# Optimization experiments

Hardware: AMD Instinct MI355X
Metric: run time of the kernel (lower is better)

Reference implementation:

```python
import jax, jax.numpy as jnp
import numpy as np

N_SAMPLES = 65536
N_OSC = 16
N_RES = 16
CPD = 16
EXPR = 2
WIN = 2048
FRAMES = 512
DEF_FRAMES = 256


def fft_convolve(a, b):
    n = a.shape[-1]
    pa = jnp.pad(a, [(0, 0)] * (a.ndim - 1) + [(0, a.shape[-1])])
    pb = jnp.pad(b, [(0, 0)] * (b.ndim - 1) + [(0, b.shape[-1])])
    spec = jnp.fft.rfft(pa, axis=-1) * jnp.fft.rfft(pb, axis=-1)
    return jnp.fft.irfft(spec, axis=-1)[..., :n]


def make_ramp(n, ramp_length=10):
    return jnp.ones(n, dtype=jnp.float32).at[:ramp_length].set(jnp.linspace(0.0, 1.0, ramp_length, dtype=jnp.float32))


def setup_inputs() -> dict:
    key = jax.random.key(0)
    ks = jax.random.split(key, 12)
    u = lambda k, shape, lo, hi: jax.random.uniform(k, shape, jnp.float32, lo, hi)
    return {
        'control_signal': jax.random.normal(ks[0], (1, 1, CPD, FRAMES), jnp.float32),
        'deformations': jax.random.normal(ks[1], (1, 1, EXPR, DEF_FRAMES), jnp.float32),
        'noise': u(ks[2], (CPD, WIN), -1.0, 1.0),
        'attack_envelopes': u(ks[3], (CPD, WIN), -1.0, 1.0),
        'router': u(ks[4], (CPD, N_RES), -1.0, 1.0),
        'mix': u(ks[5], (N_RES, 2), -1.0, 1.0),
        'gains': u(ks[6], (N_RES, 1), 0.01, 1.1),
        'damping': u(ks[7], (N_OSC, N_RES, EXPR), 0.5, 1.5),
        'mass': u(ks[8], (N_OSC, N_RES, EXPR), -2.0, 2.0),
        'tension': u(ks[9], (N_OSC, N_RES, EXPR), 4.0, 9.0),
        'initial_displacement': u(ks[10], (N_OSC, N_RES, EXPR), -1.0, 2.0),
        'amplitudes': u(ks[11], (N_OSC, N_RES, EXPR, 1), -1.0, 1.0),
    }


def _materialize_resonances(damping, mass, tension, initial_displacement, amplitudes):
    time = jnp.linspace(0.0, 10.0, N_SAMPLES, dtype=jnp.float32).reshape(1, 1, 1, N_SAMPLES)
    m = jax.nn.sigmoid(mass)[..., None]
    dmp = jax.nn.sigmoid(damping)[..., None] * 30.0
    ten = 10.0 ** tension[..., None]
    x0 = initial_displacement[..., None]
    xd = dmp / (2.0 * m)
    omega = jnp.sqrt(jnp.clip(ten - xd ** 2, 1e-12, None))
    phi = jnp.arctan2(xd * x0, x0 * omega)  # initial_velocity = 0
    a = x0 / jnp.cos(phi)
    z = a * jnp.exp(-xd * time) * jnp.cos(omega * time - phi)  # (osc, res, expr, N)
    res = jnp.sum(z * amplitudes ** 2, axis=0)  # (res, expr, N)
    res = res[None, None] * make_ramp(N_SAMPLES)  # (1,1,res,expr,N)
    return res


def _forward(control_signal, deformations, noise, attack_envelopes, router, mix, gains,
             damping, mass, tension, initial_displacement, amplitudes):
    res = _materialize_resonances(damping, mass, tension, initial_displacement, amplitudes)
    res = res / (jnp.linalg.norm(res, axis=-1, keepdims=True) + 1e-8)  # unit_norm

    # routing matmul: (b,e,frames,cpd) @ (cpd,res) -> permuted back
    routed = jnp.einsum('becf,cr->berf', control_signal, router)  # (1,1,res,frames)
    before_upsample = routed

    # sparse zero-hole upsampling
    factor = N_SAMPLES // FRAMES
    up = jnp.zeros((1, 1, N_RES, 1, N_SAMPLES), control_signal.dtype)
    up = up.at[..., ::factor].set(routed[:, :, :, None, :])

    # attack envelopes: shape == window_size fast path -> elementwise noise multiply
    impulse = attack_envelopes * noise
    impulse = jnp.pad(impulse, ((0, 0), (0, N_SAMPLES - WIN)))  # ensure_last_axis_length
    impulse = impulse.reshape(1, 1, CPD, 1, N_SAMPLES)

    routed_c = fft_convolve(impulse, up)  # (1,1,16,1,N)
    cs = jnp.sum(routed_c.reshape(1, CPD, N_SAMPLES), axis=1, keepdims=True)  # (1,1,N)

    conv = fft_convolve(routed_c, res)  # (1,1,res,expr,N)

    base = jnp.zeros_like(deformations).at[:, :, 0:1, :].set(1.0)
    d = jax.nn.softmax(base + deformations, axis=-2)  # (1,1,expr,DF)
    d = d.reshape(1, 1, 1, EXPR, DEF_FRAMES)
    d = jax.image.resize(d, (1, 1, 1, EXPR, N_SAMPLES), method='linear')

    x = jnp.sum(d * conv, axis=-2)  # (1,1,res,N)

    mixes = jax.nn.softmax(mix.reshape(1, 1, N_RES, 1, 1, 2), axis=-1)
    stacked = jnp.stack([routed_c, x.reshape(routed_c.shape)], axis=-1)  # (1,1,res,1,N,2)
    x = jnp.sum(mixes * stacked, axis=-1)  # (1,1,res,1,N)
    x = x.reshape(1, 1, N_RES, N_SAMPLES)

    summed = jnp.tanh(x * jnp.abs(gains.reshape(1, 1, N_RES, 1)))
    summed = jnp.sum(summed, axis=-2, keepdims=True)  # (1,1,1,N)
    return summed, before_upsample, cs


def reference(control_signal, deformations, noise, attack_envelopes, router, mix, gains,
              damping, mass, tension, initial_displacement, amplitudes):
    return _forward(control_signal, deformations, noise, attack_envelopes, router, mix, gains,
                    damping, mass, tension, initial_displacement, amplitudes)
```

## Files before the change

### kernel.cpp

```cpp
#include <hip/hip_runtime.h>
#include <hip/hip_bf16.h>
#include <math.h>

#define N_SAMPLES 65536
#define N_OSC 16
#define N_RES 16
#define CPD 16
#define EXPR 2
#define WIN 2048
#define FRAMES 512
#define DEF_FRAMES 256
#define NRE 32
#define R1TILE 1024
#define R1TILES (N_SAMPLES / R1TILE)

#define MBLK 4096
#define RSTRIDE 67648
#define WSZ 6176
#define NSTEP 65

#define M_RES 2048
#define M_CONV 3072
#define M_AF (M_CONV + NSTEP)
#define M_TOTAL (M_AF + 64)

typedef __hip_bfloat16 bf16;
typedef __attribute__((ext_vector_type(8))) _Float16 half8v;
typedef __attribute__((ext_vector_type(4))) float f32x4;
typedef __attribute__((ext_vector_type(4))) unsigned short ushort4v;
typedef __attribute__((ext_vector_type(8))) unsigned short ushort8v;

static __device__ __forceinline__ float ldv(const void* p, int i, int f32f) {
    if (f32f) return ((const float*)p)[i];
    return __bfloat162float(((const bf16*)p)[i]);
}
static __device__ __forceinline__ void stv(void* p, int i, float v, int f32f) {
    if (f32f) ((float*)p)[i] = v;
    else      ((bf16*)p)[i] = __float2bfloat16(v);
}
static __device__ __forceinline__ unsigned short f2h(float f) {
    union { _Float16 h; unsigned short u; } a; a.h = (_Float16)f; return a.u;
}

#define OUT_SUM_OFF 0
#define OUT_ROUTED_OFF 65536
#define OUT_CS_OFF 73728

#define DT_F64 (10.0 / 65535.0)
#define INV2PI 0.15915494309189535

__global__ __launch_bounds__(256) void prep_kernel(
    const void* ctrl, const void* defo, const void* noise, const void* attack,
    const void* router, const void* mix, const void* gains,
    const void* damping, const void* mass, const void* tension,
    const void* x0in, const void* amps,
    double* par, float* impulse, float* routed, float* dcur, float* mixg,
    int* rsup, int* nbound, int* gflag, float* sumf, void* out)
{
    int tid = threadIdx.x;
    int b = blockIdx.x;
    __shared__ int sbad;
    if (tid == 0) sbad = 0;
    __syncthreads();
    {
        const bf16* tb = (const bf16*)tension;
        int bad = 0;
        for (int i = tid; i < N_OSC * N_RES * EXPR; i += 256) {
            float v = __bfloat162float(tb[i]);
            if (!(v > 3.0f && v < 10.0f)) bad = 1;
        }
        if (bad) sbad = 1;
    }
    __syncthreads();
    const int f32f = sbad;

    if (b < 32) {
        int r = b >> 1;
        int f = ((b & 1) << 8) + tid;
        float s = 0.f;
#pragma unroll
        for (int c = 0; c < CPD; ++c)
            s += ldv(ctrl, c * FRAMES + f, f32f) * ldv(router, c * N_RES + r, f32f);
        int i = r * FRAMES + f;
        routed[i] = s;
        stv(out, OUT_ROUTED_OFF + i, s, f32f);
    } else if (b < 64) {
        int base = (b - 32) * 1024 + tid * 4;
#pragma unroll
        for (int j = 0; j < 4; ++j) {
            int i = base + j;
            impulse[i] = ldv(attack, i, f32f) * ldv(noise, i, f32f);
        }
    } else if (b == 64) {
        int i = tid;
        if (i < DEF_FRAMES) {
            float a0 = 1.0f + ldv(defo, i, f32f);
            float a1 = ldv(defo, DEF_FRAMES + i, f32f);
            float mx = fmaxf(a0, a1);
            float e0 = expf(a0 - mx), e1 = expf(a1 - mx);
            float inv = 1.0f / (e0 + e1);
            dcur[i] = e0 * inv;
            dcur[DEF_FRAMES + i] = e1 * inv;
        }
    } else if (b == 65) {
        if (tid < N_RES) {
            int r = tid;
            float a0 = ldv(mix, 2 * r, f32f), a1 = ldv(mix, 2 * r + 1, f32f);
            float mx = fmaxf(a0, a1);
            float e0 = expf(a0 - mx), e1 = expf(a1 - mx);
            float inv = 1.0f / (e0 + e1);
            mixg[r] = e0 * inv; mixg[16 + r] = e1 * inv;
            mixg[32 + r] = fabsf(ldv(gains, r, f32f));
        }
        if (tid < NRE) rsup[tid] = 0;
        if (tid == 0) gflag[0] = f32f;
    } else if (b < 98) {
        int re = b - 66;
        __shared__ double s_xd[16];
        if (tid < 16) {
            int o = tid;
            int i = o * 32 + re;
            double mm  = 1.0 / (1.0 + exp(-(double)ldv(mass, i, f32f)));
            double dmp = 30.0 / (1.0 + exp(-(double)ldv(damping, i, f32f)));
            double ten = pow(10.0, (double)ldv(tension, i, f32f));
            double x0  = (double)ldv(x0in, i, f32f);
            double amp = (double)ldv(amps, i, f32f);
            double xd  = dmp / (2.0 * mm);
            double om2 = ten - xd * xd;
            if (om2 < 1e-12) om2 = 1e-12;
            double om  = sqrt(om2);
            double phi = atan2(xd * x0, x0 * om);
            double a   = (x0 == 0.0) ? 0.0 : x0 / cos(phi);
            int p = re * 16 + o;
            par[p] = xd; par[512 + p] = om; par[1024 + p] = phi; par[1536 + p] = a * amp * amp;
            s_xd[o] = xd;
        }
        __syncthreads();
        if (tid == 0) {
            double mt = 0.0;
            for (int o = 0; o < 16; ++o) {
                double t = 35.0 / s_xd[o];
                if (t > mt) mt = t;
            }
            int nb = (int)(mt * 6553.5) + 1;
            if (nb > N_SAMPLES - 1) nb = N_SAMPLES - 1;
            nbound[re] = nb;
        }
    } else {
        ((float4*)sumf)[(b - 98) * 256 + tid] = float4{0.f, 0.f, 0.f, 0.f};
    }
}

__global__ __launch_bounds__(256) void mid_kernel(
    const double* par, const int* nbound, double* dssq_part, int* rsup,
    unsigned short* res_rev, const float* impulse, const float* routed,
    float* routed_c, unsigned short* afrag, unsigned short* rfrag)
{
    int b = blockIdx.x;
    int tid = threadIdx.x;
    if (b < M_RES) {
        int re = b >> 6, tile = b & 63;
        int n0 = tile * R1TILE;
        unsigned short* rrc = res_rev + (size_t)re * RSTRIDE;
        if (tile == R1TILES - 1) {
            ushort8v z = {0,0,0,0,0,0,0,0};
            for (int i = tid * 8; i < RSTRIDE - N_SAMPLES; i += 2048)
                *(ushort8v*)&rrc[N_SAMPLES + i] = z;
        }
        if (n0 > nbound[re]) {
            ushort8v z = {0,0,0,0,0,0,0,0};
            *(ushort8v*)&rrc[(N_SAMPLES - n0 - R1TILE) + tid * 8] = z;
            if (tid == 0) dssq_part[re * R1TILES + tile] = 0.0;
            return;
        }
        __shared__ double s_om[16], s_phi[16], s_xd[16], s_coef[16];
        __shared__ float s_drev[16], s_decf[16];
        if (tid < 16) {
            int pi = re * 16 + tid;
            double xd = par[pi], om = par[512 + pi];
            s_xd[tid] = xd; s_om[tid] = om;
            s_phi[tid] = par[1024 + pi]; s_coef[tid] = par[1536 + pi];
            s_drev[tid] = (float)(om * DT_F64 * INV2PI);
            s_decf[tid] = (float)exp(-xd * DT_F64);
        }
        __syncthreads();
        int ns = n0 + tid * 4;
        double t0 = (double)ns * DT_F64;
        float p[16], cd[16], drev[16], decf[16];
#pragma unroll
        for (int o = 0; o < 16; ++o) {
            double arg = s_om[o] * t0 - s_phi[o];
            double rev = arg * INV2PI;
            rev -= rint(rev);
            p[o] = (float)rev;
            cd[o] = (float)s_coef[o] * expf((float)(-s_xd[o] * t0));
            drev[o] = s_drev[o]; decf[o] = s_decf[o];
        }
        float vals[4];
        double ssq = 0.0;
#pragma unroll
        for (int j = 0; j < 4; ++j) {
            float acc = 0.f;
#pragma unroll
            for (int o = 0; o < 16; ++o) {
                acc += cd[o] * __builtin_amdgcn_cosf(p[o]);
                cd[o] *= decf[o];
                float pn = p[o] + drev[o];
                p[o] = pn - floorf(pn);
            }
            int n = ns + j;
            if (n < 10) acc *= (float)n * (1.0f / 9.0f);
            vals[j] = acc;
            ssq += (double)acc * (double)acc;
        }
        unsigned short u0 = f2h(vals[0]), u1 = f2h(vals[1]);
        unsigned short u2 = f2h(vals[2]), u3 = f2h(vals[3]);
        ushort4v o4 = { u3, u2, u1, u0 };
        *(ushort4v*)&rrc[(N_SAMPLES - 4) - ns] = o4;
        int mi = 0;
        if ((unsigned short)(u0 << 1)) mi = ns;
        if ((unsigned short)(u1 << 1)) mi = ns + 1;
        if ((unsigned short)(u2 << 1)) mi = ns + 2;
        if ((unsigned short)(u3 << 1)) mi = ns + 3;
        __shared__ int ib[256];
        __shared__ double rb[256];
        ib[tid] = mi; rb[tid] = ssq; __syncthreads();
        for (int st = 128; st > 0; st >>= 1) {
            if (tid < st) { ib[tid] = max(ib[tid], ib[tid + st]); rb[tid] += rb[tid + st]; }
            __syncthreads();
        }
        if (tid == 0) {
            dssq_part[re * R1TILES + tile] = rb[0];
            if (ib[0] > 0) atomicMax(&rsup[re], ib[0]);
        }
        return;
    }
    if (b < M_CONV) {
        int cb = b - M_RES;
        int c = cb >> 6;
        int n0 = (cb & 63) << 10;
        int q0 = n0 >> 7;
        __shared__ float imp_s[WIN];
        __shared__ float ro_s[24];
        {
            const float4* src = (const float4*)(impulse + c * WIN);
            float4* dst = (float4*)imp_s;
#pragma unroll
            for (int k = 0; k < 2; ++k) dst[tid + 256 * k] = src[tid + 256 * k];
            if (tid < 23) {
                int k = q0 - 15 + tid;
                ro_s[tid] = (k >= 0) ? routed[c * FRAMES + k] : 0.0f;
            }
        }
        __syncthreads();
        int s4 = (4 * tid) & 127;
        int qi = tid >> 5;
        float a0 = 0.f, a1 = 0.f, a2 = 0.f, a3 = 0.f;
#pragma unroll
        for (int dk = 0; dk < 16; ++dk) {
            float rv = ro_s[qi + 15 - dk];
            float4 iv = *(const float4*)&imp_s[s4 + (dk << 7)];
            a0 += rv * iv.x; a1 += rv * iv.y; a2 += rv * iv.z; a3 += rv * iv.w;
        }
        *(float4*)&routed_c[(size_t)c * N_SAMPLES + n0 + 4 * tid] = float4{a0, a1, a2, a3};
        return;
    }
    if (b < M_AF) {
        int t = b - M_CONV;
        for (int idx = tid; idx < 16 * 512; idx += 256) {
            int ch = idx >> 9, r = idx & 511;
            int lane = r >> 3, s = r & 7;
            int k = 32 * t + ((lane >> 4) << 3) + s - (lane & 15);
            float v = (k >= 0 && k < WIN) ? impulse[ch * WIN + k] : 0.0f;
            afrag[(size_t)((ch * NSTEP + t) * 64 + lane) * 8 + s] = f2h(v);
        }
        return;
    }
    {
        int bb = b - M_AF;
        for (int idx = bb * 4096 + tid; idx < bb * 4096 + 4096; idx += 256) {
            int ss = idx & 7, ln = (idx >> 3) & 63, v = (idx >> 9) & 31, r = idx >> 14;
            int k = 16 * v + (ln & 15) - 8 * (ln >> 4) - ss;
            float val = (k >= 0 && k < FRAMES) ? routed[r * FRAMES + k] : 0.0f;
            rfrag[idx] = f2h(val);
        }
    }
}

__global__ __launch_bounds__(256) void fir_kernel(const unsigned short* res_rev,
                                                  const unsigned short* afrag,
                                                  const int* rsup, const double* dssq_part,
                                                  unsigned short* ghT)
{
    int re = blockIdx.y;
    int mb = blockIdx.x * MBLK;
    int tid = threadIdx.x;
    int rs = rsup[re];
    int d0 = mb >> 7;
    unsigned short* ghc = ghT + (size_t)re * N_SAMPLES;
    if (mb > rs + (WIN - 1)) {
        int s = tid >> 1, h = tid & 1;
        ushort8v z = {0,0,0,0,0,0,0,0};
        size_t o = (size_t)s * 512 + d0 + 16 * h;
        *(ushort8v*)&ghc[o] = z;
        *(ushort8v*)&ghc[o + 8] = z;
        return;
    }
    __shared__ unsigned short W[WSZ];
    __shared__ double s_in[64];
    __shared__ float s_invf;
    if (tid < 64) s_in[tid] = dssq_part[re * R1TILES + tid];
    {
        const unsigned short* src = res_rev + (size_t)re * RSTRIDE + (N_SAMPLES - MBLK - mb);
        for (int i = tid * 8; i < WSZ; i += 2048)
            *(ushort8v*)&W[i] = *(const ushort8v*)&src[i];
    }
    __syncthreads();
    if (tid == 0) {
        double s = 0.0;
#pragma unroll
        for (int i = 0; i < 64; ++i) s += s_in[i];
        s_invf = (float)(1.0 / (sqrt(s) + 1e-8));
    }

    int w = tid >> 6, lane = tid & 63;
    int j = lane & 15, g = lane >> 4;
    const unsigned short* af = afrag + (size_t)(re >> 1) * (NSTEP * 512) + lane * 8;

    int c00 = mb + 1024 * w + 15;
    int c01 = c00 + 256, c02 = c00 + 512, c03 = c00 + 768;
    int tlo0 = max(0, (c00 - rs) >> 5), tlo1 = max(0, (c01 - rs) >> 5);
    int tlo2 = max(0, (c02 - rs) >> 5), tlo3 = max(0, (c03 - rs) >> 5);
    int thi0 = min(NSTEP - 1, (c00 + 240) >> 5), thi1 = min(NSTEP - 1, (c01 + 240) >> 5);
    int thi2 = min(NSTEP - 1, (c02 + 240) >> 5), thi3 = min(NSTEP - 1, (c03 + 240) >> 5);
    int tmin = tlo0, tmax = thi3;

    f32x4 acc0 = {0.f,0.f,0.f,0.f}, acc1 = acc0, acc2 = acc0, acc3 = acc0;
    int xbase = 4080 - 1024 * w - 16 * j + 8 * g;

    half8v afr = {};
    if (tmin <= tmax) afr = *(const half8v*)(af + (size_t)tmin * 512);
    for (int t = tmin; t <= tmax; ++t) {
        half8v acur = afr;
        if (t < tmax) afr = *(const half8v*)(af + (size_t)(t + 1) * 512);
        int xt = xbase + 32 * t;
        if (t >= tlo0 && t <= thi0)
            acc0 = __builtin_amdgcn_mfma_f32_16x16x32_f16(acur, *(const half8v*)&W[xt],       acc0, 0, 0, 0);
        if (t >= tlo1 && t <= thi1)
            acc1 = __builtin_amdgcn_mfma_f32_16x16x32_f16(acur, *(const half8v*)&W[xt - 256], acc1, 0, 0, 0);
        if (t >= tlo2 && t <= thi2)
            acc2 = __builtin_amdgcn_mfma_f32_16x16x32_f16(acur, *(const half8v*)&W[xt - 512], acc2, 0, 0, 0);
        if (t >= tlo3 && t <= thi3)
            acc3 = __builtin_amdgcn_mfma_f32_16x16x32_f16(acur, *(const half8v*)&W[xt - 768], acc3, 0, 0, 0);
    }

    __syncthreads();
    float invf = s_invf;
    unsigned short* T = W;
    int base_nm = 1024 * w + 16 * j + 15 - 4 * g;
#define WT(ACC, AA) { \
    int nm0_ = base_nm + 256 * (AA); \
    T[((nm0_    ) & 127) * 37 + ((nm0_    ) >> 7)] = f2h(ACC[0] * invf); \
    T[((nm0_ - 1) & 127) * 37 + ((nm0_ - 1) >> 7)] = f2h(ACC[1] * invf); \
    T[((nm0_ - 2) & 127) * 37 + ((nm0_ - 2) >> 7)] = f2h(ACC[2] * invf); \
    T[((nm0_ - 3) & 127) * 37 + ((nm0_ - 3) >> 7)] = f2h(ACC[3] * invf); }
    WT(acc0, 0) WT(acc1, 1) WT(acc2, 2) WT(acc3, 3)
#undef WT
    __syncthreads();
    {
        int s = tid >> 1, h = tid & 1;
        const unsigned short* Tr = T + s * 37 + 16 * h;
        ushort8v o0, o1;
#pragma unroll
        for (int k = 0; k < 8; ++k) { o0[k] = Tr[k]; o1[k] = Tr[8 + k]; }
        size_t o = (size_t)s * 512 + d0 + 16 * h;
        *(ushort8v*)&ghc[o] = o0;
        *(ushort8v*)&ghc[o + 8] = o1;
    }
}

__global__ __launch_bounds__(256) void conv2_kernel(const unsigned short* ghT,
        const unsigned short* rfrag, const float* routed_c, const float* dcur,
        const float* mixg, const int* rsup, float* sumf)
{
    __shared__ float xbuf[4][2048];
    __shared__ float dcur_s[2 * DEF_FRAMES];
    __shared__ float mix_s[48];
    int tid = threadIdx.x;
    int qt = blockIdx.x, rg = blockIdx.y;
    int q0 = qt * 16;
    int w = tid >> 6, lane = tid & 63;
    int j = lane & 15, gq = lane >> 4;
    int re = rg * 4 + w;
    int r = re >> 1, e = re & 1;

    if (tid < 48) mix_s[tid] = mixg[tid];
    for (int i = tid; i < 2 * DEF_FRAMES; i += 256) dcur_s[i] = dcur[i];
    __syncthreads();

    int tmax = (q0 + 15) >> 5;
    int sup = rsup[re] + (WIN - 1);
    int tend = min(tmax, sup >> 12);

    f32x4 acc[8];
#pragma unroll
    for (int st = 0; st < 8; ++st) acc[st] = f32x4{0.f, 0.f, 0.f, 0.f};

    const unsigned short* rfb = rfrag + ((size_t)r * 32 * 64 + lane) * 8;
    const unsigned short* gT = ghT + (size_t)re * N_SAMPLES;
    for (int t = 0; t <= tend; ++t) {
        int v = (q0 - 32 * t) >> 4;
        half8v a = *(const half8v*)(rfb + (size_t)v * 512);
        int bofs = j * 512 + 8 * gq + 32 * t;
#pragma unroll
        for (int st = 0; st < 8; ++st)
            acc[st] = __builtin_amdgcn_mfma_f32_16x16x32_f16(
                a, *(const half8v*)(gT + bofs + st * 8192), acc[st], 0, 0, 0);
    }

    float* xb = xbuf[w];
    const float* dc = dcur_s + DEF_FRAMES * e;
#pragma unroll
    for (int st = 0; st < 8; ++st) {
#pragma unroll
        for (int p = 0; p < 4; ++p) {
            int nl = 128 * (4 * gq + p) + 16 * st + j;
            int n = 128 * q0 + nl;
            float xc = ((float)n + 0.5f) * (1.0f / 256.0f) - 0.5f;
            float fl = floorf(xc);
            int i0 = (int)fl;
            float wfr = xc - fl;
            int ia = min(max(i0, 0), DEF_FRAMES - 1);
            int ib2 = min(max(i0 + 1, 0), DEF_FRAMES - 1);
            float de = dc[ia] * (1.0f - wfr) + dc[ib2] * wfr;
            xb[nl] = acc[st][p] * de;
        }
    }
    __syncthreads();

    int r0 = rg * 2, r1 = rg * 2 + 1;
    float m00 = mix_s[r0], m01 = mix_s[16 + r0], g0s = mix_s[32 + r0];
    float m10 = mix_s[r1], m11 = mix_s[16 + r1], g1s = mix_s[32 + r1];
    const float* rc0 = routed_c + (size_t)r0 * N_SAMPLES + 128 * q0;
    const float* rc1 = routed_c + (size_t)r1 * N_SAMPLES + 128 * q0;
    float* sf = sumf + 128 * q0;
    for (int nl = tid; nl < 2048; nl += 256) {
        float xr0 = xbuf[0][nl] + xbuf[1][nl];
        float xr1 = xbuf[2][nl] + xbuf[3][nl];
        float xf0 = m00 * rc0[nl] + m01 * xr0;
        float xf1 = m10 * rc1[nl] + m11 * xr1;
        atomicAdd(&sf[nl], tanhf(xf0 * g0s) + tanhf(xf1 * g1s));
    }
}

__global__ __launch_bounds__(256) void final2_kernel(const float* sumf, const float* routed_c,
                                                     const int* gflag, void* out)
{
    int f32f = gflag[0];
    int n = (blockIdx.x * 256 + threadIdx.x) * 4;
    float4 v = *(const float4*)(sumf + n);
    stv(out, OUT_SUM_OFF + n,     v.x, f32f);
    stv(out, OUT_SUM_OFF + n + 1, v.y, f32f);
    stv(out, OUT_SUM_OFF + n + 2, v.z, f32f);
    stv(out, OUT_SUM_OFF + n + 3, v.w, f32f);
    float c0 = 0.f, c1 = 0.f, c2 = 0.f, c3 = 0.f;
#pragma unroll
    for (int c = 0; c < CPD; ++c) {
        float4 t = *(const float4*)(routed_c + (size_t)c * N_SAMPLES + n);
        c0 += t.x; c1 += t.y; c2 += t.z; c3 += t.w;
    }
    stv(out, OUT_CS_OFF + n,     c0, f32f);
    stv(out, OUT_CS_OFF + n + 1, c1, f32f);
    stv(out, OUT_CS_OFF + n + 2, c2, f32f);
    stv(out, OUT_CS_OFF + n + 3, c3, f32f);
}

extern "C" void kernel_launch(void* const* d_in, const int* in_sizes, int n_in,
                              void* d_out, int out_size, void* d_ws, size_t ws_size,
                              hipStream_t stream)
{
    const void* ctrl    = d_in[0];
    const void* defo    = d_in[1];
    const void* noise   = d_in[2];
    const void* attack  = d_in[3];
    const void* router  = d_in[4];
    const void* mix     = d_in[5];
    const void* gains   = d_in[6];
    const void* damping = d_in[7];
    const void* mass    = d_in[8];
    const void* tension = d_in[9];
    const void* x0in    = d_in[10];
    const void* amps    = d_in[11];

    char* ws = (char*)d_ws;
    double* par       = (double*)(ws);
    double* dssq_part = (double*)(ws + 16384);
    int* gflag        = (int*)(ws + 32768);
    int* rsup         = (int*)(ws + 32896);
    int* nbound       = (int*)(ws + 33024);
    float* mixg       = (float*)(ws + 33152);
    float* dcur       = (float*)(ws + 33344);
    float* routed     = (float*)(ws + 35456);
    float* impulse    = (float*)(ws + 68224);
    unsigned short* afrag = (unsigned short*)(ws + 199296);
    unsigned short* rfrag = (unsigned short*)(ws + 1264256);
    float* sumf       = (float*)(ws + 1788544);
    unsigned short* ghT = (unsigned short*)(ws + 2097152);
    unsigned short* res_rev = (unsigned short*)(ws + 10485760);
    float* routed_c   = (float*)(ws + 14815232);

    prep_kernel<<<dim3(162), dim3(256), 0, stream>>>(
        ctrl, defo, noise, attack, router, mix, gains, damping, mass, tension,
        x0in, amps, par, impulse, routed, dcur, mixg, rsup, nbound, gflag, sumf, d_out);
    mid_kernel<<<dim3(M_TOTAL), dim3(256), 0, stream>>>(
        par, nbound, dssq_part, rsup, res_rev, impulse, routed, routed_c, afrag, rfrag);
    fir_kernel<<<dim3(N_SAMPLES / MBLK, NRE), dim3(256), 0, stream>>>(
        res_rev, afrag, rsup, dssq_part, ghT);
    conv2_kernel<<<dim3(32, 8), dim3(256), 0, stream>>>(ghT, rfrag, routed_c, dcur, mixg, rsup, sumf);
    final2_kernel<<<dim3(64), dim3(256), 0, stream>>>(sumf, routed_c, gflag, d_out);
}
```

Measured before the change: 141.2 us.

## Fuse conv and final stages, repartition conv grid over sample subtiles

The conv kernel now splits work by sample sub-stripe instead of resonance group, so each block accumulates all 16 resonances and both expressions for its outputs. The cross-block atomicAdd into a zeroed sum buffer and the separate final kernel are both removed. The block reduces partials in shared memory and writes the output and control-sum directly. Per-wave MFMA work stays similar but needs per-channel tend predicates, and each block now reads more A fragments. It saves one kernel launch, the buffer zeroing and the atomics.

```diff
diff --git a/kernel.cpp b/kernel.cpp
--- a/kernel.cpp
+++ b/kernel.cpp
@@ -55,7 +55,7 @@
     const void* damping, const void* mass, const void* tension,
     const void* x0in, const void* amps,
     double* par, float* impulse, float* routed, float* dcur, float* mixg,
-    int* rsup, int* nbound, int* gflag, float* sumf, void* out)
+    int* rsup, int* nbound, int* gflag, void* out)
 {
     int tid = threadIdx.x;
     int b = blockIdx.x;
@@ -114,7 +114,7 @@
         }
         if (tid < NRE) rsup[tid] = 0;
         if (tid == 0) gflag[0] = f32f;
-    } else if (b < 98) {
+    } else {
         int re = b - 66;
         __shared__ double s_xd[16];
         if (tid < 16) {
@@ -146,8 +146,6 @@
             if (nb > N_SAMPLES - 1) nb = N_SAMPLES - 1;
             nbound[re] = nb;
         }
-    } else {
-        ((float4*)sumf)[(b - 98) * 256 + tid] = float4{0.f, 0.f, 0.f, 0.f};
     }
 }
 
@@ -379,100 +377,112 @@
     }
 }
 
-__global__ __launch_bounds__(256) void conv2_kernel(const unsigned short* ghT,
+__global__ __launch_bounds__(256) void conv3_kernel(const unsigned short* ghT,
         const unsigned short* rfrag, const float* routed_c, const float* dcur,
-        const float* mixg, const int* rsup, float* sumf)
+        const float* mixg, const int* rsup, const int* gflag, void* out)
 {
-    __shared__ float xbuf[4][2048];
+    __shared__ float xs[4][256];
     __shared__ float dcur_s[2 * DEF_FRAMES];
     __shared__ float mix_s[48];
     int tid = threadIdx.x;
-    int qt = blockIdx.x, rg = blockIdx.y;
+    int qt = blockIdx.x, sg = blockIdx.y;
     int q0 = qt * 16;
     int w = tid >> 6, lane = tid & 63;
     int j = lane & 15, gq = lane >> 4;
-    int re = rg * 4 + w;
-    int r = re >> 1, e = re & 1;
+    int f32f = gflag[0];
 
     if (tid < 48) mix_s[tid] = mixg[tid];
     for (int i = tid; i < 2 * DEF_FRAMES; i += 256) dcur_s[i] = dcur[i];
     __syncthreads();
 
     int tmax = (q0 + 15) >> 5;
-    int sup = rsup[re] + (WIN - 1);
-    int tend = min(tmax, sup >> 12);
-
-    f32x4 acc[8];
-#pragma unroll
-    for (int st = 0; st < 8; ++st) acc[st] = f32x4{0.f, 0.f, 0.f, 0.f};
-
-    const unsigned short* rfb = rfrag + ((size_t)r * 32 * 64 + lane) * 8;
-    const unsigned short* gT = ghT + (size_t)re * N_SAMPLES;
-    for (int t = 0; t <= tend; ++t) {
+    int tend[4][2];
+    int twm = 0;
+#pragma unroll
+    for (int rr = 0; rr < 4; ++rr) {
+#pragma unroll
+        for (int e = 0; e < 2; ++e) {
+            int re = 2 * (4 * w + rr) + e;
+            int te = min(tmax, (rsup[re] + (WIN - 1)) >> 12);
+            tend[rr][e] = te;
+            twm = max(twm, te);
+        }
+    }
+
+    f32x4 acc[4][2];
+#pragma unroll
+    for (int rr = 0; rr < 4; ++rr) { acc[rr][0] = f32x4{0.f,0.f,0.f,0.f}; acc[rr][1] = f32x4{0.f,0.f,0.f,0.f}; }
+
+    const unsigned short* gTb[4][2];
+#pragma unroll
+    for (int rr = 0; rr < 4; ++rr) {
+#pragma unroll
+        for (int e = 0; e < 2; ++e) {
+            int re = 2 * (4 * w + rr) + e;
+            gTb[rr][e] = ghT + (size_t)re * N_SAMPLES + sg * 8192 + j * 512 + 8 * gq;
+        }
+    }
+
+    for (int t = 0; t <= twm; ++t) {
         int v = (q0 - 32 * t) >> 4;
-        half8v a = *(const half8v*)(rfb + (size_t)v * 512);
-        int bofs = j * 512 + 8 * gq + 32 * t;
-#pragma unroll
-        for (int st = 0; st < 8; ++st)
-            acc[st] = __builtin_amdgcn_mfma_f32_16x16x32_f16(
-                a, *(const half8v*)(gT + bofs + st * 8192), acc[st], 0, 0, 0);
-    }
-
-    float* xb = xbuf[w];
-    const float* dc = dcur_s + DEF_FRAMES * e;
-#pragma unroll
-    for (int st = 0; st < 8; ++st) {
+        int boff = 32 * t;
+        half8v a0 = *(const half8v*)(rfrag + ((size_t)(4 * w + 0) * 2048 + lane) * 8 + (size_t)v * 512);
+        half8v a1 = *(const half8v*)(rfrag + ((size_t)(4 * w + 1) * 2048 + lane) * 8 + (size_t)v * 512);
+        half8v a2 = *(const half8v*)(rfrag + ((size_t)(4 * w + 2) * 2048 + lane) * 8 + (size_t)v * 512);
+        half8v a3 = *(const half8v*)(rfrag + ((size_t)(4 * w + 3) * 2048 + lane) * 8 + (size_t)v * 512);
+#define MF(RR, AA) { \
+        if (t <= tend[RR][0]) acc[RR][0] = __builtin_amdgcn_mfma_f32_16x16x32_f16( \
+            AA, *(const half8v*)(gTb[RR][0] + boff), acc[RR][0], 0, 0, 0); \
+        if (t <= tend[RR][1]) acc[RR][1] = __builtin_amdgcn_mfma_f32_16x16x32_f16( \
+            AA, *(const half8v*)(gTb[RR][1] + boff), acc[RR][1], 0, 0, 0); }
+        MF(0, a0) MF(1, a1) MF(2, a2) MF(3, a3)
+#undef MF
+    }
+
+    float d0v[4], d1v[4];
+    int nv[4];
+#pragma unroll
+    for (int p = 0; p < 4; ++p) {
+        int n = 2048 * qt + 512 * gq + 128 * p + 16 * sg + j;
+        nv[p] = n;
+        float xc = ((float)n + 0.5f) * (1.0f / 256.0f) - 0.5f;
+        float fl = floorf(xc);
+        int i0 = (int)fl;
+        float wfr = xc - fl;
+        int ia = min(max(i0, 0), DEF_FRAMES - 1);
+        int ib2 = min(max(i0 + 1, 0), DEF_FRAMES - 1);
+        d0v[p] = dcur_s[ia] * (1.0f - wfr) + dcur_s[ib2] * wfr;
+        d1v[p] = dcur_s[DEF_FRAMES + ia] * (1.0f - wfr) + dcur_s[DEF_FRAMES + ib2] * wfr;
+    }
+
+    float part[4] = {0.f, 0.f, 0.f, 0.f};
+#pragma unroll
+    for (int rr = 0; rr < 4; ++rr) {
+        int r = 4 * w + rr;
+        float m0 = mix_s[r], m1 = mix_s[16 + r], gn = mix_s[32 + r];
+        const float* rc = routed_c + (size_t)r * N_SAMPLES;
 #pragma unroll
         for (int p = 0; p < 4; ++p) {
-            int nl = 128 * (4 * gq + p) + 16 * st + j;
-            int n = 128 * q0 + nl;
-            float xc = ((float)n + 0.5f) * (1.0f / 256.0f) - 0.5f;
-            float fl = floorf(xc);
-            int i0 = (int)fl;
-            float wfr = xc - fl;
-            int ia = min(max(i0, 0), DEF_FRAMES - 1);
-            int ib2 = min(max(i0 + 1, 0), DEF_FRAMES - 1);
-            float de = dc[ia] * (1.0f - wfr) + dc[ib2] * wfr;
-            xb[nl] = acc[st][p] * de;
-        }
-    }
-    __syncthreads();
-
-    int r0 = rg * 2, r1 = rg * 2 + 1;
-    float m00 = mix_s[r0], m01 = mix_s[16 + r0], g0s = mix_s[32 + r0];
-    float m10 = mix_s[r1], m11 = mix_s[16 + r1], g1s = mix_s[32 + r1];
-    const float* rc0 = routed_c + (size_t)r0 * N_SAMPLES + 128 * q0;
-    const float* rc1 = routed_c + (size_t)r1 * N_SAMPLES + 128 * q0;
-    float* sf = sumf + 128 * q0;
-    for (int nl = tid; nl < 2048; nl += 256) {
-        float xr0 = xbuf[0][nl] + xbuf[1][nl];
-        float xr1 = xbuf[2][nl] + xbuf[3][nl];
-        float xf0 = m00 * rc0[nl] + m01 * xr0;
-        float xf1 = m10 * rc1[nl] + m11 * xr1;
-        atomicAdd(&sf[nl], tanhf(xf0 * g0s) + tanhf(xf1 * g1s));
-    }
-}
-
-__global__ __launch_bounds__(256) void final2_kernel(const float* sumf, const float* routed_c,
-                                                     const int* gflag, void* out)
-{
-    int f32f = gflag[0];
-    int n = (blockIdx.x * 256 + threadIdx.x) * 4;
-    float4 v = *(const float4*)(sumf + n);
-    stv(out, OUT_SUM_OFF + n,     v.x, f32f);
-    stv(out, OUT_SUM_OFF + n + 1, v.y, f32f);
-    stv(out, OUT_SUM_OFF + n + 2, v.z, f32f);
-    stv(out, OUT_SUM_OFF + n + 3, v.w, f32f);
-    float c0 = 0.f, c1 = 0.f, c2 = 0.f, c3 = 0.f;
-#pragma unroll
-    for (int c = 0; c < CPD; ++c) {
-        float4 t = *(const float4*)(routed_c + (size_t)c * N_SAMPLES + n);
-        c0 += t.x; c1 += t.y; c2 += t.z; c3 += t.w;
-    }
-    stv(out, OUT_CS_OFF + n,     c0, f32f);
-    stv(out, OUT_CS_OFF + n + 1, c1, f32f);
-    stv(out, OUT_CS_OFF + n + 2, c2, f32f);
-    stv(out, OUT_CS_OFF + n + 3, c3, f32f);
+            float xmix = d0v[p] * acc[rr][0][p] + d1v[p] * acc[rr][1][p];
+            float xf = m0 * rc[nv[p]] + m1 * xmix;
+            part[p] += tanhf(xf * gn);
+        }
+    }
+#pragma unroll
+    for (int p = 0; p < 4; ++p) xs[w][(4 * gq + p) * 16 + j] = part[p];
+    __syncthreads();
+
+    {
+        int i = tid >> 4, j2 = tid & 15;
+        int n = 2048 * qt + 128 * i + 16 * sg + j2;
+        float tot = xs[0][tid] + xs[1][tid] + xs[2][tid] + xs[3][tid];
+        stv(out, OUT_SUM_OFF + n, tot, f32f);
+        float cs = 0.f;
+#pragma unroll
+        for (int c = 0; c < CPD; ++c)
+            cs += routed_c[(size_t)c * N_SAMPLES + n];
+        stv(out, OUT_CS_OFF + n, cs, f32f);
+    }
 }
 
 extern "C" void kernel_launch(void* const* d_in, const int* in_sizes, int n_in,
@@ -504,18 +514,17 @@
     float* impulse    = (float*)(ws + 68224);
     unsigned short* afrag = (unsigned short*)(ws + 199296);
     unsigned short* rfrag = (unsigned short*)(ws + 1264256);
-    float* sumf       = (float*)(ws + 1788544);
     unsigned short* ghT = (unsigned short*)(ws + 2097152);
     unsigned short* res_rev = (unsigned short*)(ws + 10485760);
     float* routed_c   = (float*)(ws + 14815232);
 
-    prep_kernel<<<dim3(162), dim3(256), 0, stream>>>(
+    prep_kernel<<<dim3(98), dim3(256), 0, stream>>>(
         ctrl, defo, noise, attack, router, mix, gains, damping, mass, tension,
-        x0in, amps, par, impulse, routed, dcur, mixg, rsup, nbound, gflag, sumf, d_out);
+        x0in, amps, par, impulse, routed, dcur, mixg, rsup, nbound, gflag, d_out);
     mid_kernel<<<dim3(M_TOTAL), dim3(256), 0, stream>>>(
         par, nbound, dssq_part, rsup, res_rev, impulse, routed, routed_c, afrag, rfrag);
     fir_kernel<<<dim3(N_SAMPLES / MBLK, NRE), dim3(256), 0, stream>>>(
         res_rev, afrag, rsup, dssq_part, ghT);
-    conv2_kernel<<<dim3(32, 8), dim3(256), 0, stream>>>(ghT, rfrag, routed_c, dcur, mixg, rsup, sumf);
-    final2_kernel<<<dim3(64), dim3(256), 0, stream>>>(sumf, routed_c, gflag, d_out);
-}
+    conv3_kernel<<<dim3(32, 8), dim3(256), 0, stream>>>(
+        ghT, rfrag, routed_c, dcur, mixg, rsup, gflag, d_out);
+}
```

Result: no change. 140.6 us (-0.4%).
